# Performance work log

Hardware: AMD Instinct MI355X
Metric: run time of the kernel (lower is better)

Reference implementation:

```python
import jax, jax.numpy as jnp
import numpy as np

D_MODEL, D_INNER, D_STATE, DT_RANK, USERS = 2560, 5120, 16, 160, 32

def setup_inputs() -> dict:
    key = jax.random.key(0)
    ks = jax.random.split(key, 16)
    s = lambda k, shp, sc=0.02: (jax.random.normal(k, shp, dtype=jnp.float32) * sc)
    return {
        "x": jax.random.normal(ks[0], (1, 1, USERS, D_MODEL), dtype=jnp.float32),
        "w_in_ssm": s(ks[1], (D_MODEL, D_INNER)),
        "w_in_mlp": s(ks[2], (D_MODEL, D_INNER)),
        "w_out": s(ks[3], (D_INNER, D_MODEL)),
        "conv_w": s(ks[4], (4, D_INNER), 0.5),
        "conv_b": s(ks[5], (D_INNER,), 0.1),
        "conv_state1": jax.random.normal(ks[6], (1, 1, USERS, D_INNER), dtype=jnp.float32),
        "conv_state2": jax.random.normal(ks[7], (1, 1, USERS, D_INNER), dtype=jnp.float32),
        "conv_state3": jax.random.normal(ks[8], (1, 1, USERS, D_INNER), dtype=jnp.float32),
        "x_proj_w": s(ks[9], (D_INNER, DT_RANK + 2 * D_STATE)),
        "dt_proj_w": s(ks[10], (DT_RANK, D_INNER)),
        "dt_proj_b": s(ks[11], (D_INNER,), 0.1),
        "A_log": jax.random.uniform(ks[12], (D_INNER, D_STATE), dtype=jnp.float32),
        "D_param": s(ks[13], (D_INNER,), 1.0),
        "ssm_state": jax.random.normal(ks[14], (USERS, D_INNER, D_STATE), dtype=jnp.float32) * 0.1,
    }

def reference(x, w_in_ssm, w_in_mlp, w_out, conv_w, conv_b,
              conv_state1, conv_state2, conv_state3,
              x_proj_w, dt_proj_w, dt_proj_b, A_log, D_param, ssm_state):
    xb = x.reshape(USERS, D_MODEL)                       # [U, d_model]
    xs = xb @ w_in_ssm                                    # [U, d_inner] (newest conv tap)
    # 4-tap depthwise causal conv via shifted state buffer (unrolled in original)
    taps = (conv_state1.reshape(USERS, D_INNER),
            conv_state2.reshape(USERS, D_INNER),
            conv_state3.reshape(USERS, D_INNER),
            xs)
    c = taps[0] * conv_w[0] + taps[1] * conv_w[1] + taps[2] * conv_w[2] + taps[3] * conv_w[3] + conv_b
    c = jax.nn.silu(c)                                    # [U, d_inner]
    # selective SSM single-step update
    x_dbl = c @ x_proj_w                                  # [U, dt_rank + 2*d_state]
    dt = jax.nn.softplus(x_dbl[:, :DT_RANK] @ dt_proj_w + dt_proj_b)   # [U, d_inner]
    B = x_dbl[:, DT_RANK:DT_RANK + D_STATE]               # [U, d_state]
    C = x_dbl[:, DT_RANK + D_STATE:]                      # [U, d_state]
    A = -jnp.exp(A_log)                                   # [d_inner, d_state]
    dA = jnp.exp(dt[:, :, None] * A[None])                # [U, d_inner, d_state]
    new_state = ssm_state * dA + (dt * c)[:, :, None] * B[:, None, :]
    y = jnp.einsum("uds,us->ud", new_state, C) + D_param * c           # [U, d_inner]
    res = xb @ w_in_mlp                                   # gate branch (no extra silu, per source)
    out = (y * res) @ w_out                               # [U, d_model]
    return out.reshape(1, 1, USERS, D_MODEL)
```

## Files before the change

kernel.cpp:

```cpp
#include <hip/hip_runtime.h>
#include <hip/hip_bf16.h>
#include <cstdint>
#include <cstddef>

#define U   32
#define DM  2560
#define DI  5120
#define DS  16
#define RNK 160
#define XD  192
#define KC1 20
#define KC4 80

typedef __attribute__((ext_vector_type(8)))  short bf16x8;
typedef __attribute__((ext_vector_type(16))) float f32x16;

__device__ __forceinline__ unsigned int pkbf(float a, float b) {
  __hip_bfloat162 h = __float22bfloat162_rn(make_float2(a, b));
  union { __hip_bfloat162 h; unsigned int u; } v; v.h = h; return v.u;
}
__device__ __forceinline__ unsigned short f2bfu(float f) {
  __hip_bfloat16 h = __float2bfloat16(f);
  union { __hip_bfloat16 h; unsigned short u; } v; v.h = h; return v.u;
}
__device__ __forceinline__ float bf2f(unsigned int s) {
  union { float f; unsigned int u; } v; v.u = s << 16; return v.f;
}

template<int LDW, int CHUNK>
__global__ __launch_bounds__(256, 4) void skinny_mfma(
    const float* __restrict__ A, int lda,
    const float* __restrict__ W0, const float* __restrict__ W1,
    unsigned short* __restrict__ part)
{
  constexpr int NS = CHUNK / 16;
  __shared__ unsigned int albuf[NS][65][4];
  __shared__ unsigned int bbuf[8][256];

  const int tid = threadIdx.x;
  const int kcb = blockIdx.y, z = blockIdx.z;
  const int k0  = kcb * CHUNK;
  const float* __restrict__ W = z ? W1 : W0;
  const int col0 = blockIdx.x * 256;

  for (int i = tid; i < U * (CHUNK / 2); i += 256) {
    const int u  = i / (CHUNK / 2);
    const int kp = i - u * (CHUNK / 2);
    const int k  = 2 * kp;
    const float2 v = *(const float2*)&A[(size_t)u * lda + k0 + k];
    albuf[k >> 4][u + U * ((k >> 3) & 1)][(k >> 1) & 3] = pkbf(v.x, v.y);
  }

  const int c4 = (tid & 63) * 4;
  const int rp = tid >> 6;
  const float* __restrict__ wb = W + ((size_t)k0 + 2 * rp) * LDW + col0 + c4;

  const int lane = tid & 63, w = tid >> 6;
  const int cl = lane & 31, half = lane >> 5;
  const int bcol = w * 64 + cl;

  f32x16 acc0{}, acc1{};

  float4 r0 = *(const float4*)(wb);
  float4 r1 = *(const float4*)(wb + LDW);
  float4 r2 = *(const float4*)(wb + (size_t)8 * LDW);
  float4 r3 = *(const float4*)(wb + (size_t)9 * LDW);

#pragma unroll
  for (int ks = 0; ks < NS; ++ks) {
    uint4 dA, dB;
    dA.x = pkbf(r0.x, r1.x); dA.y = pkbf(r0.y, r1.y);
    dA.z = pkbf(r0.z, r1.z); dA.w = pkbf(r0.w, r1.w);
    dB.x = pkbf(r2.x, r3.x); dB.y = pkbf(r2.y, r3.y);
    dB.z = pkbf(r2.z, r3.z); dB.w = pkbf(r2.w, r3.w);
    *(uint4*)&bbuf[rp][c4]     = dA;
    *(uint4*)&bbuf[rp + 4][c4] = dB;
    if (ks + 1 < NS) {
      const float* wn = wb + (size_t)(ks + 1) * 16 * LDW;
      r0 = *(const float4*)(wn);
      r1 = *(const float4*)(wn + LDW);
      r2 = *(const float4*)(wn + (size_t)8 * LDW);
      r3 = *(const float4*)(wn + (size_t)9 * LDW);
    }
    __syncthreads();
    bf16x8 af = *(const bf16x8*)&albuf[ks][lane][0];
    union { bf16x8 v; unsigned int d[4]; } b0, b1;
#pragma unroll
    for (int q = 0; q < 4; ++q) {
      b0.d[q] = bbuf[half * 4 + q][bcol];
      b1.d[q] = bbuf[half * 4 + q][bcol + 32];
    }
    acc0 = __builtin_amdgcn_mfma_f32_32x32x16_bf16(af, b0.v, acc0, 0, 0, 0);
    acc1 = __builtin_amdgcn_mfma_f32_32x32x16_bf16(af, b1.v, acc1, 0, 0, 0);
    __syncthreads();
  }

  unsigned short* po = part + (size_t)(z * gridDim.y + kcb) * U * LDW + col0;
#pragma unroll
  for (int f = 0; f < 2; ++f) {
    const int gc = w * 64 + f * 32 + cl;
    const f32x16& a = f ? acc1 : acc0;
#pragma unroll
    for (int r = 0; r < 16; ++r) {
      const int m = (r & 3) + 8 * (r >> 2) + 4 * half;
      po[(size_t)m * LDW + gc] = f2bfu(a[r]);
    }
  }
}

__global__ __launch_bounds__(256) void k2a_convsilu(
    const unsigned short* __restrict__ part,
    const float* __restrict__ cs1, const float* __restrict__ cs2,
    const float* __restrict__ cs3,
    const float* __restrict__ cw,  const float* __restrict__ cb,
    float* __restrict__ c_ws, float* __restrict__ res_ws)
{
  const int t = blockIdx.x * 256 + threadIdx.x;
  const int i = 2 * t;
  const int u = i / DI, d = i - u * DI;
  float xs0 = 0.f, xs1 = 0.f, rs0 = 0.f, rs1 = 0.f;
#pragma unroll 4
  for (int kc = 0; kc < KC1; ++kc) {
    unsigned int a = *(const unsigned int*)&part[((size_t)kc * U + u) * DI + d];
    unsigned int b = *(const unsigned int*)&part[((size_t)(KC1 + kc) * U + u) * DI + d];
    xs0 += bf2f(a & 0xffffu); xs1 += bf2f(a >> 16);
    rs0 += bf2f(b & 0xffffu); rs1 += bf2f(b >> 16);
  }
  const float2 s1 = *(const float2*)&cs1[i];
  const float2 s2 = *(const float2*)&cs2[i];
  const float2 s3 = *(const float2*)&cs3[i];
  const float2 w0 = *(const float2*)&cw[d];
  const float2 w1 = *(const float2*)&cw[DI + d];
  const float2 w2 = *(const float2*)&cw[2 * DI + d];
  const float2 w3 = *(const float2*)&cw[3 * DI + d];
  const float2 bb = *(const float2*)&cb[d];
  float c0 = s1.x * w0.x + s2.x * w1.x + s3.x * w2.x + xs0 * w3.x + bb.x;
  float c1 = s1.y * w0.y + s2.y * w1.y + s3.y * w2.y + xs1 * w3.y + bb.y;
  c0 = c0 / (1.f + __expf(-c0));
  c1 = c1 / (1.f + __expf(-c1));
  *(float2*)&c_ws[i]   = make_float2(c0, c1);
  *(float2*)&res_ws[i] = make_float2(rs0, rs1);
}

__global__ __launch_bounds__(256) void k2b_xproj(
    const float* __restrict__ c_ws,
    const float* __restrict__ xpw,
    float* __restrict__ x_dbl)
{
  __shared__ union { float ct[U][80]; float red[4][64][33]; } sh;
  const int k0 = blockIdx.y * 80;

  for (int i4 = threadIdx.x; i4 < U * 20; i4 += 256) {
    int u = i4 / 20, k4 = i4 - u * 20;
    *(float4*)&sh.ct[u][k4 * 4] = *(const float4*)&c_ws[u * DI + k0 + k4 * 4];
  }
  __syncthreads();

  const int c = threadIdx.x & 63, s = threadIdx.x >> 6;
  const int col = blockIdx.x * 64 + c;
  const float* Wp = xpw + (size_t)(k0 + s * 20) * XD + col;

  float acc[U];
#pragma unroll
  for (int u = 0; u < U; ++u) acc[u] = 0.f;

  for (int kk = 0; kk < 20; kk += 4) {
    float w0 = Wp[(size_t)(kk + 0) * XD];
    float w1 = Wp[(size_t)(kk + 1) * XD];
    float w2 = Wp[(size_t)(kk + 2) * XD];
    float w3 = Wp[(size_t)(kk + 3) * XD];
#pragma unroll
    for (int u = 0; u < U; ++u) {
      float4 cv = *(const float4*)&sh.ct[u][s * 20 + kk];
      acc[u] = fmaf(cv.x, w0, acc[u]);
      acc[u] = fmaf(cv.y, w1, acc[u]);
      acc[u] = fmaf(cv.z, w2, acc[u]);
      acc[u] = fmaf(cv.w, w3, acc[u]);
    }
  }

  __syncthreads();
#pragma unroll
  for (int u = 0; u < U; ++u) sh.red[s][c][u] = acc[u];
  __syncthreads();

  for (int p = threadIdx.x; p < 64 * U; p += 256) {
    int cc = p & 63, u = p >> 6;
    float v = sh.red[0][cc][u] + sh.red[1][cc][u] + sh.red[2][cc][u] + sh.red[3][cc][u];
    atomicAdd(&x_dbl[u * XD + blockIdx.x * 64 + cc], v);
  }
}

__global__ __launch_bounds__(256) void k3a_dt(
    const float* __restrict__ x_dbl,
    const float* __restrict__ dpw, const float* __restrict__ dpb,
    float* __restrict__ dt_ws)
{
  __shared__ union { float xt[U][160]; float red[4][64][33]; } sh;

  for (int i4 = threadIdx.x; i4 < U * 40; i4 += 256) {
    int u = i4 / 40, r4 = i4 - u * 40;
    *(float4*)&sh.xt[u][r4 * 4] = *(const float4*)&x_dbl[u * XD + r4 * 4];
  }
  __syncthreads();

  const int c = threadIdx.x & 63, s = threadIdx.x >> 6;
  const int d = blockIdx.x * 64 + c;
  const float* Wp = dpw + (size_t)(s * 40) * DI + d;

  float acc[U];
#pragma unroll
  for (int u = 0; u < U; ++u) acc[u] = 0.f;

  for (int rr = 0; rr < 40; rr += 4) {
    float w0 = Wp[(size_t)(rr + 0) * DI];
    float w1 = Wp[(size_t)(rr + 1) * DI];
    float w2 = Wp[(size_t)(rr + 2) * DI];
    float w3 = Wp[(size_t)(rr + 3) * DI];
#pragma unroll
    for (int u = 0; u < U; ++u) {
      float4 xv = *(const float4*)&sh.xt[u][s * 40 + rr];
      acc[u] = fmaf(xv.x, w0, acc[u]);
      acc[u] = fmaf(xv.y, w1, acc[u]);
      acc[u] = fmaf(xv.z, w2, acc[u]);
      acc[u] = fmaf(xv.w, w3, acc[u]);
    }
  }

  __syncthreads();
#pragma unroll
  for (int u = 0; u < U; ++u) sh.red[s][c][u] = acc[u];
  __syncthreads();

  for (int p = threadIdx.x; p < 64 * U; p += 256) {
    int cc = p & 63, u = p >> 6;
    int dg = blockIdx.x * 64 + cc;
    float pre = sh.red[0][cc][u] + sh.red[1][cc][u] + sh.red[2][cc][u] + sh.red[3][cc][u]
              + dpb[dg];
    float dt = fmaxf(pre, 0.f) + log1pf(expf(-fabsf(pre)));
    dt_ws[u * DI + dg] = dt;
  }
}

__global__ __launch_bounds__(256) void k3b_ssm(
    const float* __restrict__ x_dbl,
    const float* __restrict__ alog, const float* __restrict__ Dp,
    const float* __restrict__ ssm,
    const float* __restrict__ dt_ws,
    const float* __restrict__ c_ws, const float* __restrict__ res_ws,
    float* __restrict__ yr)
{
  const int i = blockIdx.x * 256 + threadIdx.x;
  const int u = i / DI, d = i - u * DI;

  const float dt = dt_ws[i];
  const float cv = c_ws[i];
  const float rv = res_ws[i];
  const float Dv = Dp[d];
  const float dtc = dt * cv;

  float4 B[4], C[4];
#pragma unroll
  for (int q = 0; q < 4; ++q) {
    B[q] = *(const float4*)&x_dbl[u * XD + RNK + q * 4];
    C[q] = *(const float4*)&x_dbl[u * XD + RNK + DS + q * 4];
  }

  const float* st = ssm + ((size_t)u * DI + d) * DS;
  float y = 0.f;
#pragma unroll
  for (int q = 0; q < 4; ++q) {
    float4 al = *(const float4*)&alog[d * DS + q * 4];
    float4 sv = *(const float4*)&st[q * 4];
    y += (sv.x * __expf(dt * -__expf(al.x)) + dtc * B[q].x) * C[q].x;
    y += (sv.y * __expf(dt * -__expf(al.y)) + dtc * B[q].y) * C[q].y;
    y += (sv.z * __expf(dt * -__expf(al.z)) + dtc * B[q].z) * C[q].z;
    y += (sv.w * __expf(dt * -__expf(al.w)) + dtc * B[q].w) * C[q].w;
  }
  y = fmaf(Dv, cv, y);
  yr[i] = y * rv;
}

__global__ __launch_bounds__(256) void k5_reduce(
    const unsigned short* __restrict__ part4,
    float* __restrict__ out)
{
  const int t = blockIdx.x * 256 + threadIdx.x;
  const int i = 2 * t;
  const int u = i / DM, d = i - u * DM;
  float v0 = 0.f, v1 = 0.f;
#pragma unroll 8
  for (int kc = 0; kc < KC4; ++kc) {
    unsigned int a = *(const unsigned int*)&part4[((size_t)kc * U + u) * DM + d];
    v0 += bf2f(a & 0xffffu);
    v1 += bf2f(a >> 16);
  }
  *(float2*)&out[i] = make_float2(v0, v1);
}

extern "C" void kernel_launch(void* const* d_in, const int* in_sizes, int n_in,
                              void* d_out, int out_size, void* d_ws, size_t ws_size,
                              hipStream_t stream)
{
  const float* x    = (const float*)d_in[0];
  const float* wssm = (const float*)d_in[1];
  const float* wmlp = (const float*)d_in[2];
  const float* wout = (const float*)d_in[3];
  const float* cw   = (const float*)d_in[4];
  const float* cb   = (const float*)d_in[5];
  const float* cs1  = (const float*)d_in[6];
  const float* cs2  = (const float*)d_in[7];
  const float* cs3  = (const float*)d_in[8];
  const float* xpw  = (const float*)d_in[9];
  const float* dpw  = (const float*)d_in[10];
  const float* dpb  = (const float*)d_in[11];
  const float* alog = (const float*)d_in[12];
  const float* Dp   = (const float*)d_in[13];
  const float* ssm  = (const float*)d_in[14];
  float* out = (float*)d_out;

  unsigned short* partb = (unsigned short*)d_ws;
  float* c_ws   = (float*)(partb + (size_t)2 * KC1 * U * DI);
  float* res_ws = c_ws   + (size_t)U * DI;
  float* dt_ws  = res_ws + (size_t)U * DI;
  float* yrb    = dt_ws  + (size_t)U * DI;
  float* x_dbl  = yrb    + (size_t)U * DI;

  (void)hipMemsetAsync(x_dbl, 0, (size_t)U * XD * sizeof(float), stream);

  skinny_mfma<DI, 128><<<dim3(20, KC1, 2), 256, 0, stream>>>(x, DM, wssm, wmlp, partb);
  k2a_convsilu<<<320, 256, 0, stream>>>(partb, cs1, cs2, cs3, cw, cb, c_ws, res_ws);
  k2b_xproj<<<dim3(3, 64), 256, 0, stream>>>(c_ws, xpw, x_dbl);
  k3a_dt<<<80, 256, 0, stream>>>(x_dbl, dpw, dpb, dt_ws);
  k3b_ssm<<<640, 256, 0, stream>>>(x_dbl, alog, Dp, ssm, dt_ws, c_ws, res_ws, yrb);
  skinny_mfma<DM, 64><<<dim3(10, KC4, 1), 256, 0, stream>>>(yrb, DI, wout, wout, partb);
  k5_reduce<<<160, 256, 0, stream>>>(partb, out);
}
```

Before: 84.97 us.

## Stream weights via global_load_lds double buffering with larger K slabs

```diff
diff --git a/kernel.cpp b/kernel.cpp
--- a/kernel.cpp
+++ b/kernel.cpp
@@ -9,8 +9,8 @@
 #define DS  16
 #define RNK 160
 #define XD  192
-#define KC1 20
-#define KC4 80
+#define KC1 8
+#define KC4 32
 
 typedef __attribute__((ext_vector_type(8)))  short bf16x8;
 typedef __attribute__((ext_vector_type(16))) float f32x16;
@@ -27,79 +27,86 @@
   union { float f; unsigned int u; } v; v.u = s << 16; return v.f;
 }
 
-template<int LDW, int CHUNK>
-__global__ __launch_bounds__(256, 4) void skinny_mfma(
+__device__ __forceinline__ void gl_lds16(const float* g, float* l) {
+  __builtin_amdgcn_global_load_lds(
+      (const __attribute__((address_space(1))) unsigned int*)g,
+      (__attribute__((address_space(3))) unsigned int*)l,
+      16, 0, 0);
+}
+
+template<int LDW, int SLAB>
+__global__ __launch_bounds__(256, 3) void skinny_dma(
     const float* __restrict__ A, int lda,
     const float* __restrict__ W0, const float* __restrict__ W1,
     unsigned short* __restrict__ part)
 {
-  constexpr int NS = CHUNK / 16;
-  __shared__ unsigned int albuf[NS][65][4];
-  __shared__ unsigned int bbuf[8][256];
-
-  const int tid = threadIdx.x;
-  const int kcb = blockIdx.y, z = blockIdx.z;
-  const int k0  = kcb * CHUNK;
+  constexpr int NS = SLAB / 16;
+  __shared__ float        wbuf[2][16][256];
+  __shared__ unsigned int albuf[NS][64][4];
+
+  const int tid  = threadIdx.x;
+  const int lane = tid & 63, w = tid >> 6;
+  const int kcb  = blockIdx.y, z = blockIdx.z;
+  const int k0   = kcb * SLAB;
   const float* __restrict__ W = z ? W1 : W0;
   const int col0 = blockIdx.x * 256;
 
-  for (int i = tid; i < U * (CHUNK / 2); i += 256) {
-    const int u  = i / (CHUNK / 2);
-    const int kp = i - u * (CHUNK / 2);
+  for (int i = tid; i < U * (SLAB / 2); i += 256) {
+    const int u  = i / (SLAB / 2);
+    const int kp = i - u * (SLAB / 2);
     const int k  = 2 * kp;
     const float2 v = *(const float2*)&A[(size_t)u * lda + k0 + k];
     albuf[k >> 4][u + U * ((k >> 3) & 1)][(k >> 1) & 3] = pkbf(v.x, v.y);
   }
 
-  const int c4 = (tid & 63) * 4;
-  const int rp = tid >> 6;
-  const float* __restrict__ wb = W + ((size_t)k0 + 2 * rp) * LDW + col0 + c4;
-
-  const int lane = tid & 63, w = tid >> 6;
   const int cl = lane & 31, half = lane >> 5;
-  const int bcol = w * 64 + cl;
+
+  {
+    const float* src = W + ((size_t)k0 + w * 4) * LDW + col0 + lane * 4;
+#pragma unroll
+    for (int i = 0; i < 4; ++i)
+      gl_lds16(src + (size_t)i * LDW, &wbuf[0][w * 4 + i][0]);
+  }
 
   f32x16 acc0{}, acc1{};
 
-  float4 r0 = *(const float4*)(wb);
-  float4 r1 = *(const float4*)(wb + LDW);
-  float4 r2 = *(const float4*)(wb + (size_t)8 * LDW);
-  float4 r3 = *(const float4*)(wb + (size_t)9 * LDW);
-
-#pragma unroll
-  for (int ks = 0; ks < NS; ++ks) {
-    uint4 dA, dB;
-    dA.x = pkbf(r0.x, r1.x); dA.y = pkbf(r0.y, r1.y);
-    dA.z = pkbf(r0.z, r1.z); dA.w = pkbf(r0.w, r1.w);
-    dB.x = pkbf(r2.x, r3.x); dB.y = pkbf(r2.y, r3.y);
-    dB.z = pkbf(r2.z, r3.z); dB.w = pkbf(r2.w, r3.w);
-    *(uint4*)&bbuf[rp][c4]     = dA;
-    *(uint4*)&bbuf[rp + 4][c4] = dB;
-    if (ks + 1 < NS) {
-      const float* wn = wb + (size_t)(ks + 1) * 16 * LDW;
-      r0 = *(const float4*)(wn);
-      r1 = *(const float4*)(wn + LDW);
-      r2 = *(const float4*)(wn + (size_t)8 * LDW);
-      r3 = *(const float4*)(wn + (size_t)9 * LDW);
+  for (int s = 0; s < NS; ++s) {
+    const int buf = s & 1;
+    if (s + 1 < NS) {
+      const float* src = W + ((size_t)k0 + (s + 1) * 16 + w * 4) * LDW
+                         + col0 + lane * 4;
+#pragma unroll
+      for (int i = 0; i < 4; ++i)
+        gl_lds16(src + (size_t)i * LDW, &wbuf[buf ^ 1][w * 4 + i][0]);
     }
     __syncthreads();
-    bf16x8 af = *(const bf16x8*)&albuf[ks][lane][0];
-    union { bf16x8 v; unsigned int d[4]; } b0, b1;
-#pragma unroll
-    for (int q = 0; q < 4; ++q) {
-      b0.d[q] = bbuf[half * 4 + q][bcol];
-      b1.d[q] = bbuf[half * 4 + q][bcol + 32];
-    }
-    acc0 = __builtin_amdgcn_mfma_f32_32x32x16_bf16(af, b0.v, acc0, 0, 0, 0);
-    acc1 = __builtin_amdgcn_mfma_f32_32x32x16_bf16(af, b1.v, acc1, 0, 0, 0);
+
+    bf16x8 af = *(const bf16x8*)&albuf[s][lane][0];
+#pragma unroll
+    for (int f = 0; f < 2; ++f) {
+      const int col = w * 64 + f * 32 + cl;
+      float r0 = wbuf[buf][half * 8 + 0][col];
+      float r1 = wbuf[buf][half * 8 + 1][col];
+      float r2 = wbuf[buf][half * 8 + 2][col];
+      float r3 = wbuf[buf][half * 8 + 3][col];
+      float r4 = wbuf[buf][half * 8 + 4][col];
+      float r5 = wbuf[buf][half * 8 + 5][col];
+      float r6 = wbuf[buf][half * 8 + 6][col];
+      float r7 = wbuf[buf][half * 8 + 7][col];
+      union { bf16x8 v; unsigned int d[4]; } bu;
+      bu.d[0] = pkbf(r0, r1); bu.d[1] = pkbf(r2, r3);
+      bu.d[2] = pkbf(r4, r5); bu.d[3] = pkbf(r6, r7);
+      if (f == 0) acc0 = __builtin_amdgcn_mfma_f32_32x32x16_bf16(af, bu.v, acc0, 0, 0, 0);
+      else        acc1 = __builtin_amdgcn_mfma_f32_32x32x16_bf16(af, bu.v, acc1, 0, 0, 0);
+    }
     __syncthreads();
   }
 
   unsigned short* po = part + (size_t)(z * gridDim.y + kcb) * U * LDW + col0;
 #pragma unroll
   for (int f = 0; f < 2; ++f) {
+    const f32x16& a = f ? acc1 : acc0;
     const int gc = w * 64 + f * 32 + cl;
-    const f32x16& a = f ? acc1 : acc0;
 #pragma unroll
     for (int r = 0; r < 16; ++r) {
       const int m = (r & 3) + 8 * (r >> 2) + 4 * half;
@@ -119,7 +126,7 @@
   const int i = 2 * t;
   const int u = i / DI, d = i - u * DI;
   float xs0 = 0.f, xs1 = 0.f, rs0 = 0.f, rs1 = 0.f;
-#pragma unroll 4
+#pragma unroll
   for (int kc = 0; kc < KC1; ++kc) {
     unsigned int a = *(const unsigned int*)&part[((size_t)kc * U + u) * DI + d];
     unsigned int b = *(const unsigned int*)&part[((size_t)(KC1 + kc) * U + u) * DI + d];
@@ -289,7 +296,7 @@
   const int i = 2 * t;
   const int u = i / DM, d = i - u * DM;
   float v0 = 0.f, v1 = 0.f;
-#pragma unroll 8
+#pragma unroll
   for (int kc = 0; kc < KC4; ++kc) {
     unsigned int a = *(const unsigned int*)&part4[((size_t)kc * U + u) * DM + d];
     v0 += bf2f(a & 0xffffu);
@@ -328,11 +335,11 @@
 
   (void)hipMemsetAsync(x_dbl, 0, (size_t)U * XD * sizeof(float), stream);
 
-  skinny_mfma<DI, 128><<<dim3(20, KC1, 2), 256, 0, stream>>>(x, DM, wssm, wmlp, partb);
+  skinny_dma<DI, 320><<<dim3(20, KC1, 2), 256, 0, stream>>>(x, DM, wssm, wmlp, partb);
   k2a_convsilu<<<320, 256, 0, stream>>>(partb, cs1, cs2, cs3, cw, cb, c_ws, res_ws);
   k2b_xproj<<<dim3(3, 64), 256, 0, stream>>>(c_ws, xpw, x_dbl);
   k3a_dt<<<80, 256, 0, stream>>>(x_dbl, dpw, dpb, dt_ws);
   k3b_ssm<<<640, 256, 0, stream>>>(x_dbl, alog, Dp, ssm, dt_ws, c_ws, res_ws, yrb);
-  skinny_mfma<DM, 64><<<dim3(10, KC4, 1), 256, 0, stream>>>(yrb, DI, wout, wout, partb);
+  skinny_dma<DM, 160><<<dim3(10, KC4, 1), 256, 0, stream>>>(yrb, DI, wout, wout, partb);
   k5_reduce<<<160, 256, 0, stream>>>(partb, out);
 }
```

Result: faster. 82.03 us (-3.5%).
